# Optimization experiments

Measured on AMD Instinct MI355X. Metric: run time of the kernel, lower is better.

The kernel has to match this reference:

```python
import jax, jax.numpy as jnp
import numpy as np

B, S, D = 8, 2048, 512


def setup_inputs() -> dict:
    root = jax.random.key(0)
    kq, kk, kv, km = jax.random.split(root, 4)
    query = jax.random.normal(kq, (B, S, D), dtype=jnp.float32)
    key = jax.random.normal(kk, (B, S, D), dtype=jnp.float32)
    value = jax.random.normal(kv, (B, S, D), dtype=jnp.float32)
    # padding mask (batch, key_len): 1 = attend, 0 = masked. Force position 0
    # valid so no causal row is entirely masked (would yield NaN softmax).
    attention_mask = jax.random.randint(km, (B, S), 0, 2, dtype=jnp.int32).at[:, 0].set(1)
    return {"query": query, "key": key, "value": value, "attention_mask": attention_mask}


def reference(query, key, value, attention_mask):
    q_len, k_len = query.shape[1], key.shape[1]
    scale = 1.0 / jnp.sqrt(jnp.asarray(key.shape[-1], dtype=query.dtype))
    # [B, q_len, k_len] scores
    scores = jnp.einsum("bqd,bkd->bqk", query, key) * scale
    # causal (mask_future=True): lower-triangular allowed
    causal = jnp.tril(jnp.ones((q_len, k_len), dtype=bool))
    scores = jnp.where(causal[None, :, :], scores, -jnp.inf)
    # padding mask broadcast over query axis: (B, 1, k_len)
    scores = jnp.where(attention_mask[:, None, :] == 0, -jnp.inf, scores)
    probs = jax.nn.softmax(scores, axis=-1)
    return jnp.einsum("bqk,bkd->bqd", probs, value)
```

## Files before the change

kernel.cpp:

```cpp
#include <hip/hip_runtime.h>
#include <hip/hip_bf16.h>


typedef short bf16x8 __attribute__((ext_vector_type(8)));
typedef short s4v    __attribute__((ext_vector_type(4)));
typedef float f32x4  __attribute__((ext_vector_type(4)));
typedef float f4v    __attribute__((ext_vector_type(4)));
typedef float f2v    __attribute__((ext_vector_type(2)));
typedef unsigned int u32;

#define DEVINL __device__ __forceinline__

constexpr int kS = 2048;
constexpr int kD = 512;
constexpr int kB = 8;
constexpr int QT = 32;
constexpr int KROW = kD + 8;
constexpr float kC = 1.4426950408889634f * 0.044194173824159216f;
constexpr size_t kSlotB = (size_t)64 * kD * 2 + 64 * 4;

DEVINL float fast_exp2(float x) {
  float r; asm("v_exp_f32 %0, %1" : "=v"(r) : "v"(x)); return r;
}
DEVINL short f2b(float f) {
  return (short)__builtin_bit_cast(unsigned short, __float2bfloat16(f));
}
DEVINL f32x4 mfma16(bf16x8 a, bf16x8 b, f32x4 c) {
  return __builtin_amdgcn_mfma_f32_16x16x32_bf16(a, b, c, 0, 0, 0);
}
DEVINL void gl_lds16(const void* g, void* l) {
  __builtin_amdgcn_global_load_lds(
      (const __attribute__((address_space(1))) u32*)g,
      (__attribute__((address_space(3))) u32*)l, 16, 0, 0);
}
DEVINL float bflo(u32 u) { return __builtin_bit_cast(float, u << 16); }
DEVINL float bfhi(u32 u) { return __builtin_bit_cast(float, u & 0xffff0000u); }

template <int CTRL>
DEVINL float mvdpp(float x) {
  return __builtin_bit_cast(float,
      __builtin_amdgcn_mov_dpp(__builtin_bit_cast(int, x), CTRL, 0xf, 0xf, false));
}
DEVINL float rowsum16(float x) {
  x += mvdpp<0x128>(x);
  x += mvdpp<0x124>(x);
  x += mvdpp<0x122>(x);
  x += mvdpp<0x121>(x);
  return x;
}

__host__ __device__ __forceinline__ int ncM(int q, int TT) {
  return (2 * q + 2 + TT - 1) / TT;
}

__global__ __launch_bounds__(256) void prep(
    const float* __restrict__ K, const float* __restrict__ V,
    short* __restrict__ Kb, short* __restrict__ Vt) {
  __shared__ float Tl[64][65];
  const int blk = blockIdx.x;
  if (blk < 1024) {
    const size_t n4 = (size_t)kB * kS * kD / 4;
    for (size_t i = (size_t)blk * 256 + threadIdx.x; i < n4;
         i += (size_t)1024 * 256) {
      f4v v = *(const f4v*)(K + i * 4);
      s4v o = {f2b(v[0]), f2b(v[1]), f2b(v[2]), f2b(v[3])};
      *(s4v*)(Kb + i * 4) = o;
    }
  } else {
    const int r = blk - 1024;
    const int b = r >> 8, rr = r & 255;
    const int s0 = (rr >> 3) * 64, d0 = (rr & 7) * 64;
    const int t = threadIdx.x;
#pragma unroll
    for (int i = 0; i < 4; ++i) {
      int v = t + i * 256;
      int row = v >> 4, cq = v & 15;
      f4v x = *(const f4v*)(V + ((size_t)(b * kS + s0 + row)) * kD + d0 + cq * 4);
      *(f4v*)&Tl[row][cq * 4] = x;
    }
    __syncthreads();
    const int dd = t >> 2, q = t & 3;
    short out[16];
#pragma unroll
    for (int j = 0; j < 16; ++j) out[j] = f2b(Tl[q * 16 + j][dd]);
    short* dp = Vt + ((size_t)(b * kD + d0 + dd)) * kS + s0 + q * 16;
    *(bf16x8*)dp = *(const bf16x8*)&out[0];
    *(bf16x8*)(dp + 8) = *(const bf16x8*)&out[8];
  }
}

__global__ __launch_bounds__(256, 2) void attn_p1(
    const float* __restrict__ Qp, const short* __restrict__ Kb,
    const short* __restrict__ Vt, const int* __restrict__ Mp,
    float* __restrict__ Op, char* __restrict__ Part, int TT, int NS) {
  __shared__ __align__(16) short Klds[32 * 512];
  __shared__ __align__(16) short Vlds[128 * 128];
  __shared__ __align__(16) short Plds[64 * 40];
  __shared__ float Llds[64];
  __shared__ unsigned char Mlds[kS];

  const int tid = threadIdx.x, lane = tid & 63, w = tid >> 6;
  const int b = blockIdx.x & 7;

  int j = blockIdx.x >> 3;
  int sub = 0, qt = 0;
  for (;;) {
    const int qmin = (sub * TT) >> 1;
    const int cnt = QT - qmin;
    if (j < cnt) { qt = (QT - 1) - j; break; }
    j -= cnt;
    ++sub;
  }
  const int nc = ncM(qt, TT);
  const int ntl = 2 * qt + 2;
  const int t0 = sub * TT, t1 = min(ntl, t0 + TT);
  const int qbase = qt * 64;

  for (int i = tid; i < kS; i += 256) Mlds[i] = (unsigned char)Mp[(size_t)b * kS + i];

  const int l15 = lane & 15, lg = lane >> 4;

  bf16x8 qa[16];
  {
    const float* qp = Qp + ((size_t)(b * kS) + qbase + w * 16 + l15) * kD + lg * 8;
#pragma unroll
    for (int k = 0; k < 16; ++k) {
      f4v a = *(const f4v*)(qp + k * 32);
      f4v c = *(const f4v*)(qp + k * 32 + 4);
      bf16x8 q8 = {f2b(a[0]), f2b(a[1]), f2b(a[2]), f2b(a[3]),
                   f2b(c[0]), f2b(c[1]), f2b(c[2]), f2b(c[3])};
      qa[k] = q8;
    }
  }

  f32x4 acc[4][8];
#pragma unroll
  for (int qb = 0; qb < 4; ++qb)
#pragma unroll
    for (int db = 0; db < 8; ++db) acc[qb][db] = f32x4{0.f, 0.f, 0.f, 0.f};
  float lsum[4] = {0.f, 0.f, 0.f, 0.f};

  const int kx4 = (l15 >> 2) & 1;
  const short* kbase2 = &Klds[l15 * 512 + ((lg ^ (l15 & 3)) << 3)];
  const short* kpE = kbase2 + (kx4 << 5);
  const short* kpO = kbase2 - (kx4 << 5);
  const int vcom = (l15 >> 2) * 128 + ((l15 >> 1) & 1) * 64 + ((lg ^ (l15 >> 2)) << 3);
  const short* vE = &Vlds[vcom + (l15 & 1) * 32];
  const short* vO = &Vlds[vcom + ((l15 & 1) ^ 1) * 32];

  for (int t = t0; t < t1; ++t) {
    const int kv0 = t * 32;
    __syncthreads();

    {
      const short* kb = Kb + ((size_t)(b * kS) + kv0) * kD;
      const short* vt = Vt + (size_t)(b * kD) * kS + kv0;
      const int li = lane & 15, lh = lane >> 4;
#pragma unroll
      for (int r8 = 0; r8 < 8; ++r8) {
        const int row = w * 8 + r8;
        gl_lds16(kb + (size_t)row * kD + ((lane ^ (row & 7)) << 3),
                 &Klds[row * 512]);
      }
#pragma unroll
      for (int r8 = 0; r8 < 8; ++r8) {
        const int i = w * 8 + r8;
        const int sr = 4 * i + lh;
        const int logical = li ^ (4 * (i & 1) + lh);
        const int d = sr * 4 + (logical >> 2);
        gl_lds16(vt + (size_t)d * kS + ((logical & 3) << 3), &Vlds[i * 512]);
      }
    }
    __syncthreads();

    f32x4 sA = {0.f,0.f,0.f,0.f}, sB = {0.f,0.f,0.f,0.f};
    f32x4 sC = {0.f,0.f,0.f,0.f}, sD = {0.f,0.f,0.f,0.f};
    __builtin_amdgcn_s_setprio(1);
#pragma unroll
    for (int k = 0; k < 16; k += 2) {
      const short* pa = kpE + (k << 5);
      const short* pb = kpO + ((k + 1) << 5);
      bf16x8 b00 = *(const bf16x8*)(pa);
      bf16x8 b10 = *(const bf16x8*)(pa + 16 * 512);
      bf16x8 b01 = *(const bf16x8*)(pb);
      bf16x8 b11 = *(const bf16x8*)(pb + 16 * 512);
      sA = mfma16(qa[k], b00, sA);
      sB = mfma16(qa[k], b10, sB);
      sC = mfma16(qa[k + 1], b01, sC);
      sD = mfma16(qa[k + 1], b11, sD);
    }
    __builtin_amdgcn_s_setprio(0);
    f32x4 s0 = sA + sC;
    f32x4 s1 = sB + sD;

    const int kvg0 = kv0 + l15, kvg1 = kvg0 + 16;
    const int mk0 = Mlds[kvg0], mk1 = Mlds[kvg1];
    const int qrow0 = qbase + w * 16 + lg * 4;
#pragma unroll
    for (int jx = 0; jx < 4; ++jx) {
      const int q = qrow0 + jx;
      float x0 = (kvg0 <= q && mk0 != 0) ? s0[jx] : -1e30f;
      float x1 = (kvg1 <= q && mk1 != 0) ? s1[jx] : -1e30f;
      float p0 = fast_exp2(x0 * kC);
      float p1 = fast_exp2(x1 * kC);
      lsum[jx] += rowsum16(p0 + p1);
      Plds[(w * 16 + lg * 4 + jx) * 40 + l15]      = f2b(p0);
      Plds[(w * 16 + lg * 4 + jx) * 40 + 16 + l15] = f2b(p1);
    }
    __syncthreads();

    __builtin_amdgcn_s_setprio(1);
#pragma unroll
    for (int half = 0; half < 2; ++half) {
      bf16x8 vf[4];
#pragma unroll
      for (int i = 0; i < 4; ++i) {
        const int dc = 8 * w + half * 4 + i;
        vf[i] = (i & 1) ? *(const bf16x8*)(vO + dc * 512)
                        : *(const bf16x8*)(vE + dc * 512);
      }
#pragma unroll
      for (int qb = 0; qb < 4; ++qb) {
        bf16x8 pa = *(const bf16x8*)&Plds[(qb * 16 + l15) * 40 + lg * 8];
#pragma unroll
        for (int i = 0; i < 4; ++i)
          acc[qb][half * 4 + i] = mfma16(pa, vf[i], acc[qb][half * 4 + i]);
      }
    }
    __builtin_amdgcn_s_setprio(0);
  }

  __syncthreads();
  if (l15 == 0) {
    f32x4 lv = {lsum[0], lsum[1], lsum[2], lsum[3]};
    *(f32x4*)&Llds[w * 16 + lg * 4] = lv;
  }
  __syncthreads();

  if (nc == 1) {
#pragma unroll
    for (int qb = 0; qb < 4; ++qb) {
      f32x4 lv = *(const f32x4*)&Llds[qb * 16 + lg * 4];
#pragma unroll
      for (int jx = 0; jx < 4; ++jx) {
        const float inv = __builtin_amdgcn_rcpf(lv[jx]);
        const int row = qbase + qb * 16 + lg * 4 + jx;
        float* op = Op + ((size_t)(b * kS) + row) * kD + w * 128 + l15;
#pragma unroll
        for (int db = 0; db < 8; ++db) op[db * 16] = acc[qb][db][jx] * inv;
      }
    }
  } else {
    int sb = 0;
    for (int q = 0; q < qt; ++q) {
      int n2 = ncM(q, TT);
      if (n2 > 1) sb += n2;
    }
    char* sp = Part + ((size_t)b * NS + sb + sub) * kSlotB;
    short* po = (short*)sp;
    float* pm = (float*)(sp + (size_t)64 * kD * 2);
#pragma unroll
    for (int qb = 0; qb < 4; ++qb) {
#pragma unroll
      for (int jx = 0; jx < 4; ++jx) {
        const int row = qb * 16 + lg * 4 + jx;
#pragma unroll
        for (int db = 0; db < 8; ++db)
          po[row * kD + w * 128 + db * 16 + l15] = f2b(acc[qb][db][jx]);
      }
    }
    if (l15 == 0) {
#pragma unroll
      for (int jx = 0; jx < 4; ++jx) pm[w * 16 + lg * 4 + jx] = lsum[jx];
    }
  }
}

__global__ __launch_bounds__(256) void attn_p2(const char* __restrict__ Part,
                                               float* __restrict__ Op,
                                               int TT, int NS) {
  const int bid = blockIdx.x;
  const int b = bid & 7, rg = (bid >> 3) & 7, idx = bid >> 6;
  int seen = 0, qt = 0, nc = 0, sbase = 0, sb = 0;
  for (int q = 0; q < QT; ++q) {
    int n2 = ncM(q, TT);
    if (n2 > 1) {
      if (seen == idx) { qt = q; nc = n2; sbase = sb; break; }
      seen++;
      sb += n2;
    }
  }
  const int t = threadIdx.x;
  const char* base = Part + ((size_t)b * NS + sbase) * kSlotB;
  const int r0 = rg * 8;
  for (int row = r0; row < r0 + 8; ++row) {
    float lt = 0.f;
    for (int c = 0; c < nc; ++c)
      lt += *(const float*)(base + c * kSlotB + 65536 + row * 4);
    const float inv = 1.0f / lt;
    float a0 = 0.f, a1 = 0.f;
    for (int c = 0; c < nc; ++c) {
      u32 u = *(const u32*)(base + c * kSlotB + ((size_t)row * kD + t * 2) * 2);
      a0 += bflo(u);
      a1 += bfhi(u);
    }
    f2v o = {a0 * inv, a1 * inv};
    *(f2v*)(Op + ((size_t)(b * kS) + qt * 64 + row) * kD + t * 2) = o;
  }
}

__global__ __launch_bounds__(256) void attn_legacy(
    const float* __restrict__ Qp, const float* __restrict__ Kp,
    const float* __restrict__ Vp, const int* __restrict__ Mp,
    float* __restrict__ Op) {
  __shared__ __align__(16) short Klds[32 * KROW];
  __shared__ __align__(16) short Vlds[32 * kD];
  __shared__ __align__(16) short Plds[4 * 16 * 40];
  __shared__ int Mlds[kS];
  const int tid = threadIdx.x, lane = tid & 63, w = tid >> 6;
  const int bb = blockIdx.x & 7, qt = blockIdx.x >> 3, qb = qt * 64;
  for (int i = tid; i < kS; i += 256) Mlds[i] = Mp[(size_t)bb * kS + i];
  const int l15 = lane & 15, lg = lane >> 4;
  bf16x8 qa[16];
  {
    const float* qp = Qp + ((size_t)bb * kS + qb + w * 16 + l15) * kD + lg * 8;
#pragma unroll
    for (int k = 0; k < 16; ++k) {
      f4v a = *(const f4v*)(qp + k * 32);
      f4v c = *(const f4v*)(qp + k * 32 + 4);
      bf16x8 q8 = {f2b(a[0]), f2b(a[1]), f2b(a[2]), f2b(a[3]),
                   f2b(c[0]), f2b(c[1]), f2b(c[2]), f2b(c[3])};
      qa[k] = q8;
    }
  }
  f32x4 acc[32];
#pragma unroll
  for (int dc = 0; dc < 32; ++dc) acc[dc] = f32x4{0.f, 0.f, 0.f, 0.f};
  float mrow[4] = {-1e30f, -1e30f, -1e30f, -1e30f};
  float lsum[4] = {0.f, 0.f, 0.f, 0.f};
  short* Pl = &Plds[w * 16 * 40];
  const int vphys = ((lg ^ ((lane >> 2) & 3)) * 16);
  const int nt = 2 * qt + 2;
  for (int t = 0; t < nt; ++t) {
    const int kv0 = t * 32;
    __syncthreads();
    {
      const int r = tid >> 3, dg = tid & 7;
      const float* src = Kp + ((size_t)bb * kS + kv0 + r) * kD + dg * 64;
      short* dst = &Klds[r * KROW + dg * 64];
#pragma unroll
      for (int i = 0; i < 16; ++i) {
        f4v v = *(const f4v*)(src + i * 4);
        s4v s = {f2b(v[0]), f2b(v[1]), f2b(v[2]), f2b(v[3])};
        *(s4v*)(dst + i * 4) = s;
      }
    }
    {
      const int kvq = tid & 7, dqi = tid >> 3;
      const float* vbase = Vp + ((size_t)bb * kS + kv0 + kvq * 4) * kD;
#pragma unroll
      for (int it = 0; it < 4; ++it) {
        const int dq = dqi + 32 * it;
        f4v v0 = *(const f4v*)(vbase + 0 * kD + dq * 4);
        f4v v1 = *(const f4v*)(vbase + 1 * kD + dq * 4);
        f4v v2 = *(const f4v*)(vbase + 2 * kD + dq * 4);
        f4v v3 = *(const f4v*)(vbase + 3 * kD + dq * 4);
        const int pch = (((kvq >> 1) ^ (dq & 3)) * 16) + (kvq & 1) * 8;
#pragma unroll
        for (int c = 0; c < 4; ++c) {
          s4v s = {f2b(v0[c]), f2b(v1[c]), f2b(v2[c]), f2b(v3[c])};
          *(s4v*)((char*)Vlds + (dq * 4 + c) * 64 + pch) = s;
        }
      }
    }
    __syncthreads();
    f32x4 sA = {0.f,0.f,0.f,0.f}, sB = {0.f,0.f,0.f,0.f};
    f32x4 sC = {0.f,0.f,0.f,0.f}, sD = {0.f,0.f,0.f,0.f};
    const short* krow0 = &Klds[l15 * KROW + lg * 8];
    const short* krow1 = krow0 + 16 * KROW;
#pragma unroll
    for (int k = 0; k < 16; k += 2) {
      bf16x8 b00 = *(const bf16x8*)(krow0 + k * 32);
      bf16x8 b10 = *(const bf16x8*)(krow1 + k * 32);
      bf16x8 b01 = *(const bf16x8*)(krow0 + (k + 1) * 32);
      bf16x8 b11 = *(const bf16x8*)(krow1 + (k + 1) * 32);
      sA = mfma16(qa[k], b00, sA);
      sB = mfma16(qa[k], b10, sB);
      sC = mfma16(qa[k + 1], b01, sC);
      sD = mfma16(qa[k + 1], b11, sD);
    }
    f32x4 s0 = sA + sC, s1 = sB + sD;
    const int kvg0 = kv0 + l15, kvg1 = kvg0 + 16;
    const int mk0 = Mlds[kvg0], mk1 = Mlds[kvg1];
    const int qrow0 = qb + w * 16 + lg * 4;
    float rm[4];
#pragma unroll
    for (int jx = 0; jx < 4; ++jx) {
      const int q = qrow0 + jx;
      float x0 = (kvg0 <= q && mk0 != 0) ? s0[jx] : -1e30f;
      float x1 = (kvg1 <= q && mk1 != 0) ? s1[jx] : -1e30f;
      s0[jx] = x0; s1[jx] = x1;
      rm[jx] = fmaxf(x0, x1);
    }
#pragma unroll
    for (int sh = 1; sh <= 8; sh <<= 1) {
#pragma unroll
      for (int jx = 0; jx < 4; ++jx) rm[jx] = fmaxf(rm[jx], __shfl_xor(rm[jx], sh));
    }
    bool need = false;
#pragma unroll
    for (int jx = 0; jx < 4; ++jx) need |= ((rm[jx] - mrow[jx]) * kC > 8.0f);
    if (__any(need)) {
#pragma unroll
      for (int jx = 0; jx < 4; ++jx) {
        float mn = fmaxf(mrow[jx], rm[jx]);
        float corr = fast_exp2((mrow[jx] - mn) * kC);
        mrow[jx] = mn;
        lsum[jx] *= corr;
#pragma unroll
        for (int dc = 0; dc < 32; ++dc) acc[dc][jx] *= corr;
      }
    }
    float ts[4];
#pragma unroll
    for (int jx = 0; jx < 4; ++jx) {
      float p0 = fast_exp2((s0[jx] - mrow[jx]) * kC);
      float p1 = fast_exp2((s1[jx] - mrow[jx]) * kC);
      ts[jx] = p0 + p1;
      Pl[(lg * 4 + jx) * 40 + l15]      = f2b(p0);
      Pl[(lg * 4 + jx) * 40 + 16 + l15] = f2b(p1);
    }
#pragma unroll
    for (int sh = 1; sh <= 8; sh <<= 1) {
#pragma unroll
      for (int jx = 0; jx < 4; ++jx) ts[jx] += __shfl_xor(ts[jx], sh);
    }
#pragma unroll
    for (int jx = 0; jx < 4; ++jx) lsum[jx] += ts[jx];
    bf16x8 pf = *(const bf16x8*)&Pl[l15 * 40 + lg * 8];
#pragma unroll
    for (int dc = 0; dc < 32; ++dc) {
      const bf16x8 vf = *(const bf16x8*)((const char*)Vlds + (dc * 16 + l15) * 64 + vphys);
      acc[dc] = mfma16(pf, vf, acc[dc]);
    }
  }
#pragma unroll
  for (int jx = 0; jx < 4; ++jx) {
    const float inv = __builtin_amdgcn_rcpf(lsum[jx]);
    float* op = Op + ((size_t)bb * kS + qb + w * 16 + lg * 4 + jx) * kD + l15;
#pragma unroll
    for (int dc = 0; dc < 32; ++dc) op[dc * 16] = acc[dc][jx] * inv;
  }
}

extern "C" void kernel_launch(void* const* d_in, const int* in_sizes, int n_in,
                              void* d_out, int out_size, void* d_ws, size_t ws_size,
                              hipStream_t stream) {
  const float* Q = (const float*)d_in[0];
  const float* K = (const float*)d_in[1];
  const float* V = (const float*)d_in[2];
  const int*   M = (const int*)d_in[3];
  float* O = (float*)d_out;

  const size_t tens = (size_t)kB * kS * kD;
  const size_t convB = 2 * tens * 2;

  if (ws_size < convB) {
    attn_legacy<<<dim3(256), dim3(256), 0, stream>>>(Q, K, V, M, O);
    return;
  }

  short* Kb = (short*)d_ws;
  short* Vt = Kb + tens;
  char* Part = (char*)d_ws + convB;
  const size_t budget = ws_size - convB;

  int TT = 68;
  {
    const int cands[5] = {12, 16, 22, 34, 48};
    for (int ci = 0; ci < 5; ++ci) {
      int tt = cands[ci], slots = 0;
      for (int q = 0; q < QT; ++q) {
        int nc = ncM(q, tt);
        if (nc > 1) slots += nc;
      }
      if ((size_t)kB * slots * kSlotB <= budget) { TT = tt; break; }
    }
  }
  int NS = 0, NCH = 0, nsplit = 0;
  for (int q = 0; q < QT; ++q) {
    int nc = ncM(q, TT);
    NCH += nc;
    if (nc > 1) { NS += nc; nsplit++; }
  }

  prep<<<dim3(3072), dim3(256), 0, stream>>>(K, V, Kb, Vt);
  attn_p1<<<dim3(kB * NCH), dim3(256), 0, stream>>>(Q, Kb, Vt, M, O, Part, TT, NS);
  if (nsplit > 0)
    attn_p2<<<dim3(kB * 8 * nsplit), dim3(256), 0, stream>>>(Part, O, TT, NS);
}
```

Measured before the change: 180.4 us.

## Shrink query tile to 32 rows, split head dim across waves, share K/V LDS

The attention kernel now processes 32-query tiles instead of 64. The four waves are arranged as 2 query blocks by 2 head-dim halves, and the partial QK scores from the two halves are exchanged through a small LDS buffer. K and V now share one LDS buffer, loaded one after the other within each tile iteration, with explicit waitcnt and barriers. The mask is read from global memory instead of being staged in LDS. This cuts LDS usage so three blocks fit per CU and gives finer work granularity, at the cost of more barriers per tile, bf16 rounding of the exchanged partial scores, and twice the K/V tile loads per query.

```diff
diff --git a/kernel.cpp b/kernel.cpp
--- a/kernel.cpp
+++ b/kernel.cpp
@@ -8,16 +8,17 @@
 typedef float f4v    __attribute__((ext_vector_type(4)));
 typedef float f2v    __attribute__((ext_vector_type(2)));
 typedef unsigned int u32;
+typedef unsigned short u16;
 
 #define DEVINL __device__ __forceinline__
 
 constexpr int kS = 2048;
 constexpr int kD = 512;
 constexpr int kB = 8;
-constexpr int QT = 32;
+constexpr int QT3 = 64;
 constexpr int KROW = kD + 8;
 constexpr float kC = 1.4426950408889634f * 0.044194173824159216f;
-constexpr size_t kSlotB = (size_t)64 * kD * 2 + 64 * 4;
+constexpr size_t kSlot3 = (size_t)32 * kD * 2 + 32 * 4;
 
 DEVINL float fast_exp2(float x) {
   float r; asm("v_exp_f32 %0, %1" : "=v"(r) : "v"(x)); return r;
@@ -25,6 +26,7 @@
 DEVINL short f2b(float f) {
   return (short)__builtin_bit_cast(unsigned short, __float2bfloat16(f));
 }
+DEVINL float b2f(u16 u) { return __builtin_bit_cast(float, (u32)u << 16); }
 DEVINL f32x4 mfma16(bf16x8 a, bf16x8 b, f32x4 c) {
   return __builtin_amdgcn_mfma_f32_16x16x32_bf16(a, b, c, 0, 0, 0);
 }
@@ -49,8 +51,8 @@
   return x;
 }
 
-__host__ __device__ __forceinline__ int ncM(int q, int TT) {
-  return (2 * q + 2 + TT - 1) / TT;
+__host__ __device__ __forceinline__ int nc3(int qt, int TT) {
+  return (qt + 1 + TT - 1) / TT;
 }
 
 __global__ __launch_bounds__(256) void prep(
@@ -89,42 +91,39 @@
   }
 }
 
-__global__ __launch_bounds__(256, 2) void attn_p1(
+__global__ __launch_bounds__(256, 3) void attn_p1(
     const float* __restrict__ Qp, const short* __restrict__ Kb,
     const short* __restrict__ Vt, const int* __restrict__ Mp,
     float* __restrict__ Op, char* __restrict__ Part, int TT, int NS) {
-  __shared__ __align__(16) short Klds[32 * 512];
-  __shared__ __align__(16) short Vlds[128 * 128];
-  __shared__ __align__(16) short Plds[64 * 40];
-  __shared__ float Llds[64];
-  __shared__ unsigned char Mlds[kS];
+  __shared__ __align__(16) short KV[32 * 512];
+  __shared__ __align__(16) short Plds[32 * 40];
+  __shared__ __align__(16) short Slds[2][2][16][32];
 
   const int tid = threadIdx.x, lane = tid & 63, w = tid >> 6;
+  const int qb2 = w & 1, dh = w >> 1;
   const int b = blockIdx.x & 7;
 
-  int j = blockIdx.x >> 3;
-  int sub = 0, qt = 0;
+  int j = blockIdx.x >> 3, sub = 0, qt = 0;
   for (;;) {
-    const int qmin = (sub * TT) >> 1;
-    const int cnt = QT - qmin;
-    if (j < cnt) { qt = (QT - 1) - j; break; }
+    const int qmin = sub * TT;
+    const int cnt = QT3 - qmin;
+    if (j < cnt) { qt = (QT3 - 1) - j; break; }
     j -= cnt;
     ++sub;
   }
-  const int nc = ncM(qt, TT);
-  const int ntl = 2 * qt + 2;
+  const int ntl = qt + 1;
+  const int nc = nc3(qt, TT);
   const int t0 = sub * TT, t1 = min(ntl, t0 + TT);
-  const int qbase = qt * 64;
-
-  for (int i = tid; i < kS; i += 256) Mlds[i] = (unsigned char)Mp[(size_t)b * kS + i];
+  const int qbase = qt * 32;
 
   const int l15 = lane & 15, lg = lane >> 4;
 
-  bf16x8 qa[16];
+  bf16x8 qa[8];
   {
-    const float* qp = Qp + ((size_t)(b * kS) + qbase + w * 16 + l15) * kD + lg * 8;
-#pragma unroll
-    for (int k = 0; k < 16; ++k) {
+    const float* qp =
+        Qp + ((size_t)(b * kS) + qbase + qb2 * 16 + l15) * kD + dh * 256 + lg * 8;
+#pragma unroll
+    for (int k = 0; k < 8; ++k) {
       f4v a = *(const f4v*)(qp + k * 32);
       f4v c = *(const f4v*)(qp + k * 32 + 4);
       bf16x8 q8 = {f2b(a[0]), f2b(a[1]), f2b(a[2]), f2b(a[3]),
@@ -133,51 +132,47 @@
     }
   }
 
-  f32x4 acc[4][8];
-#pragma unroll
-  for (int qb = 0; qb < 4; ++qb)
-#pragma unroll
-    for (int db = 0; db < 8; ++db) acc[qb][db] = f32x4{0.f, 0.f, 0.f, 0.f};
+  f32x4 acc[16];
+#pragma unroll
+  for (int dc = 0; dc < 16; ++dc) acc[dc] = f32x4{0.f, 0.f, 0.f, 0.f};
   float lsum[4] = {0.f, 0.f, 0.f, 0.f};
 
   const int kx4 = (l15 >> 2) & 1;
-  const short* kbase2 = &Klds[l15 * 512 + ((lg ^ (l15 & 3)) << 3)];
+  const short* kbase2 = &KV[l15 * 512 + dh * 256 + ((lg ^ (l15 & 3)) << 3)];
   const short* kpE = kbase2 + (kx4 << 5);
   const short* kpO = kbase2 - (kx4 << 5);
   const int vcom = (l15 >> 2) * 128 + ((l15 >> 1) & 1) * 64 + ((lg ^ (l15 >> 2)) << 3);
-  const short* vE = &Vlds[vcom + (l15 & 1) * 32];
-  const short* vO = &Vlds[vcom + ((l15 & 1) ^ 1) * 32];
+  const short* vE = &KV[vcom + (l15 & 1) * 32];
+  const short* vO = &KV[vcom + ((l15 & 1) ^ 1) * 32];
+
+  const short* kbG = Kb + (size_t)(b * kS) * kD;
+  const short* vtG = Vt + (size_t)(b * kD) * kS;
+  const int* mp = Mp + (size_t)b * kS;
 
   for (int t = t0; t < t1; ++t) {
     const int kv0 = t * 32;
-    __syncthreads();
+
+    __builtin_amdgcn_s_barrier();
+    __builtin_amdgcn_sched_barrier(0);
 
     {
-      const short* kb = Kb + ((size_t)(b * kS) + kv0) * kD;
-      const short* vt = Vt + (size_t)(b * kD) * kS + kv0;
-      const int li = lane & 15, lh = lane >> 4;
+      const short* kb = kbG + (size_t)kv0 * kD;
 #pragma unroll
       for (int r8 = 0; r8 < 8; ++r8) {
         const int row = w * 8 + r8;
         gl_lds16(kb + (size_t)row * kD + ((lane ^ (row & 7)) << 3),
-                 &Klds[row * 512]);
-      }
-#pragma unroll
-      for (int r8 = 0; r8 < 8; ++r8) {
-        const int i = w * 8 + r8;
-        const int sr = 4 * i + lh;
-        const int logical = li ^ (4 * (i & 1) + lh);
-        const int d = sr * 4 + (logical >> 2);
-        gl_lds16(vt + (size_t)d * kS + ((logical & 3) << 3), &Vlds[i * 512]);
-      }
-    }
-    __syncthreads();
+                 &KV[row * 512]);
+      }
+    }
+    asm volatile("s_waitcnt vmcnt(0)" ::: "memory");
+    __builtin_amdgcn_s_barrier();
+    __builtin_amdgcn_sched_barrier(0);
 
     f32x4 sA = {0.f,0.f,0.f,0.f}, sB = {0.f,0.f,0.f,0.f};
     f32x4 sC = {0.f,0.f,0.f,0.f}, sD = {0.f,0.f,0.f,0.f};
     __builtin_amdgcn_s_setprio(1);
 #pragma unroll
-    for (int k = 0; k < 16; k += 2) {
+    for (int k = 0; k < 8; k += 2) {
       const short* pa = kpE + (k << 5);
       const short* pb = kpO + ((k + 1) << 5);
       bf16x8 b00 = *(const bf16x8*)(pa);
@@ -190,88 +185,96 @@
       sD = mfma16(qa[k + 1], b11, sD);
     }
     __builtin_amdgcn_s_setprio(0);
-    f32x4 s0 = sA + sC;
-    f32x4 s1 = sB + sD;
-
-    const int kvg0 = kv0 + l15, kvg1 = kvg0 + 16;
-    const int mk0 = Mlds[kvg0], mk1 = Mlds[kvg1];
-    const int qrow0 = qbase + w * 16 + lg * 4;
+    f32x4 s0p = sA + sC;
+    f32x4 s1p = sB + sD;
+
 #pragma unroll
     for (int jx = 0; jx < 4; ++jx) {
-      const int q = qrow0 + jx;
-      float x0 = (kvg0 <= q && mk0 != 0) ? s0[jx] : -1e30f;
-      float x1 = (kvg1 <= q && mk1 != 0) ? s1[jx] : -1e30f;
-      float p0 = fast_exp2(x0 * kC);
-      float p1 = fast_exp2(x1 * kC);
-      lsum[jx] += rowsum16(p0 + p1);
-      Plds[(w * 16 + lg * 4 + jx) * 40 + l15]      = f2b(p0);
-      Plds[(w * 16 + lg * 4 + jx) * 40 + 16 + l15] = f2b(p1);
-    }
-    __syncthreads();
-
+      Slds[qb2][dh][lg * 4 + jx][l15]      = f2b(s0p[jx]);
+      Slds[qb2][dh][lg * 4 + jx][l15 + 16] = f2b(s1p[jx]);
+    }
+    asm volatile("s_waitcnt lgkmcnt(0)" ::: "memory");
+    __builtin_amdgcn_s_barrier();
+    __builtin_amdgcn_sched_barrier(0);
+
+    {
+      const short* vt = vtG + kv0;
+      const int li = lane & 15, lh = lane >> 4;
+#pragma unroll
+      for (int r8 = 0; r8 < 8; ++r8) {
+        const int i = w * 8 + r8;
+        const int sr = 4 * i + lh;
+        const int logical = li ^ (4 * (i & 1) + lh);
+        const int d = sr * 4 + (logical >> 2);
+        gl_lds16(vt + (size_t)d * kS + ((logical & 3) << 3), &KV[i * 512]);
+      }
+    }
+
+    {
+      const int kvg0 = kv0 + l15, kvg1 = kvg0 + 16;
+      const int mk0 = mp[kvg0], mk1 = mp[kvg1];
+      const int qrow0 = qbase + qb2 * 16 + lg * 4;
+#pragma unroll
+      for (int jx = 0; jx < 4; ++jx) {
+        const int row = lg * 4 + jx;
+        const float o0 = b2f((u16)Slds[qb2][dh ^ 1][row][l15]);
+        const float o1 = b2f((u16)Slds[qb2][dh ^ 1][row][l15 + 16]);
+        float x0 = s0p[jx] + o0;
+        float x1 = s1p[jx] + o1;
+        const int q = qrow0 + jx;
+        x0 = (kvg0 <= q && mk0 != 0) ? x0 : -1e30f;
+        x1 = (kvg1 <= q && mk1 != 0) ? x1 : -1e30f;
+        const float p0 = fast_exp2(x0 * kC);
+        const float p1 = fast_exp2(x1 * kC);
+        lsum[jx] += rowsum16(p0 + p1);
+        if (dh == 0) {
+          Plds[(qb2 * 16 + row) * 40 + l15]      = f2b(p0);
+          Plds[(qb2 * 16 + row) * 40 + 16 + l15] = f2b(p1);
+        }
+      }
+    }
+    asm volatile("s_waitcnt vmcnt(0) lgkmcnt(0)" ::: "memory");
+    __builtin_amdgcn_s_barrier();
+    __builtin_amdgcn_sched_barrier(0);
+
+    bf16x8 pa = *(const bf16x8*)&Plds[(qb2 * 16 + l15) * 40 + lg * 8];
     __builtin_amdgcn_s_setprio(1);
 #pragma unroll
-    for (int half = 0; half < 2; ++half) {
-      bf16x8 vf[4];
-#pragma unroll
-      for (int i = 0; i < 4; ++i) {
-        const int dc = 8 * w + half * 4 + i;
-        vf[i] = (i & 1) ? *(const bf16x8*)(vO + dc * 512)
-                        : *(const bf16x8*)(vE + dc * 512);
-      }
-#pragma unroll
-      for (int qb = 0; qb < 4; ++qb) {
-        bf16x8 pa = *(const bf16x8*)&Plds[(qb * 16 + l15) * 40 + lg * 8];
-#pragma unroll
-        for (int i = 0; i < 4; ++i)
-          acc[qb][half * 4 + i] = mfma16(pa, vf[i], acc[qb][half * 4 + i]);
-      }
+    for (int dc2 = 0; dc2 < 16; dc2 += 2) {
+      const int dcA = dh * 16 + dc2;
+      bf16x8 vf0 = *(const bf16x8*)(vE + dcA * 512);
+      bf16x8 vf1 = *(const bf16x8*)(vO + (dcA + 1) * 512);
+      acc[dc2]     = mfma16(pa, vf0, acc[dc2]);
+      acc[dc2 + 1] = mfma16(pa, vf1, acc[dc2 + 1]);
     }
     __builtin_amdgcn_s_setprio(0);
   }
 
-  __syncthreads();
-  if (l15 == 0) {
-    f32x4 lv = {lsum[0], lsum[1], lsum[2], lsum[3]};
-    *(f32x4*)&Llds[w * 16 + lg * 4] = lv;
-  }
-  __syncthreads();
-
   if (nc == 1) {
 #pragma unroll
-    for (int qb = 0; qb < 4; ++qb) {
-      f32x4 lv = *(const f32x4*)&Llds[qb * 16 + lg * 4];
-#pragma unroll
-      for (int jx = 0; jx < 4; ++jx) {
-        const float inv = __builtin_amdgcn_rcpf(lv[jx]);
-        const int row = qbase + qb * 16 + lg * 4 + jx;
-        float* op = Op + ((size_t)(b * kS) + row) * kD + w * 128 + l15;
-#pragma unroll
-        for (int db = 0; db < 8; ++db) op[db * 16] = acc[qb][db][jx] * inv;
-      }
+    for (int jx = 0; jx < 4; ++jx) {
+      const float inv = __builtin_amdgcn_rcpf(lsum[jx]);
+      const int row = qbase + qb2 * 16 + lg * 4 + jx;
+      float* op = Op + ((size_t)(b * kS) + row) * kD + dh * 256 + l15;
+#pragma unroll
+      for (int dc = 0; dc < 16; ++dc) op[dc * 16] = acc[dc][jx] * inv;
     }
   } else {
     int sb = 0;
     for (int q = 0; q < qt; ++q) {
-      int n2 = ncM(q, TT);
+      int n2 = nc3(q, TT);
       if (n2 > 1) sb += n2;
     }
-    char* sp = Part + ((size_t)b * NS + sb + sub) * kSlotB;
+    char* sp = Part + ((size_t)b * NS + sb + sub) * kSlot3;
     short* po = (short*)sp;
-    float* pm = (float*)(sp + (size_t)64 * kD * 2);
-#pragma unroll
-    for (int qb = 0; qb < 4; ++qb) {
-#pragma unroll
-      for (int jx = 0; jx < 4; ++jx) {
-        const int row = qb * 16 + lg * 4 + jx;
-#pragma unroll
-        for (int db = 0; db < 8; ++db)
-          po[row * kD + w * 128 + db * 16 + l15] = f2b(acc[qb][db][jx]);
-      }
-    }
-    if (l15 == 0) {
-#pragma unroll
-      for (int jx = 0; jx < 4; ++jx) pm[w * 16 + lg * 4 + jx] = lsum[jx];
+    float* pm = (float*)(sp + (size_t)32 * kD * 2);
+#pragma unroll
+    for (int jx = 0; jx < 4; ++jx) {
+      const int row = qb2 * 16 + lg * 4 + jx;
+#pragma unroll
+      for (int dc = 0; dc < 16; ++dc)
+        po[row * kD + dh * 256 + dc * 16 + l15] = f2b(acc[dc][jx]);
+      if (dh == 0 && l15 == 0) pm[row] = lsum[jx];
     }
   }
 }
@@ -280,10 +283,10 @@
                                                float* __restrict__ Op,
                                                int TT, int NS) {
   const int bid = blockIdx.x;
-  const int b = bid & 7, rg = (bid >> 3) & 7, idx = bid >> 6;
+  const int b = bid & 7, rg = (bid >> 3) & 3, idx = bid >> 5;
   int seen = 0, qt = 0, nc = 0, sbase = 0, sb = 0;
-  for (int q = 0; q < QT; ++q) {
-    int n2 = ncM(q, TT);
+  for (int q = 0; q < QT3; ++q) {
+    int n2 = nc3(q, TT);
     if (n2 > 1) {
       if (seen == idx) { qt = q; nc = n2; sbase = sb; break; }
       seen++;
@@ -291,21 +294,21 @@
     }
   }
   const int t = threadIdx.x;
-  const char* base = Part + ((size_t)b * NS + sbase) * kSlotB;
+  const char* base = Part + ((size_t)b * NS + sbase) * kSlot3;
   const int r0 = rg * 8;
   for (int row = r0; row < r0 + 8; ++row) {
     float lt = 0.f;
     for (int c = 0; c < nc; ++c)
-      lt += *(const float*)(base + c * kSlotB + 65536 + row * 4);
+      lt += *(const float*)(base + c * kSlot3 + 32768 + row * 4);
     const float inv = 1.0f / lt;
     float a0 = 0.f, a1 = 0.f;
     for (int c = 0; c < nc; ++c) {
-      u32 u = *(const u32*)(base + c * kSlotB + ((size_t)row * kD + t * 2) * 2);
+      u32 u = *(const u32*)(base + c * kSlot3 + ((size_t)row * kD + t * 2) * 2);
       a0 += bflo(u);
       a1 += bfhi(u);
     }
     f2v o = {a0 * inv, a1 * inv};
-    *(f2v*)(Op + ((size_t)(b * kS) + qt * 64 + row) * kD + t * 2) = o;
+    *(f2v*)(Op + ((size_t)(b * kS) + qt * 32 + row) * kD + t * 2) = o;
   }
 }
 
@@ -475,21 +478,21 @@
   char* Part = (char*)d_ws + convB;
   const size_t budget = ws_size - convB;
 
-  int TT = 68;
+  int TT = QT3;
   {
-    const int cands[5] = {12, 16, 22, 34, 48};
-    for (int ci = 0; ci < 5; ++ci) {
+    const int cands[4] = {16, 24, 32, 48};
+    for (int ci = 0; ci < 4; ++ci) {
       int tt = cands[ci], slots = 0;
-      for (int q = 0; q < QT; ++q) {
-        int nc = ncM(q, tt);
+      for (int q = 0; q < QT3; ++q) {
+        int nc = nc3(q, tt);
         if (nc > 1) slots += nc;
       }
-      if ((size_t)kB * slots * kSlotB <= budget) { TT = tt; break; }
+      if ((size_t)kB * slots * kSlot3 <= budget) { TT = tt; break; }
     }
   }
   int NS = 0, NCH = 0, nsplit = 0;
-  for (int q = 0; q < QT; ++q) {
-    int nc = ncM(q, TT);
+  for (int q = 0; q < QT3; ++q) {
+    int nc = nc3(q, TT);
     NCH += nc;
     if (nc > 1) { NS += nc; nsplit++; }
   }
@@ -497,5 +500,5 @@
   prep<<<dim3(3072), dim3(256), 0, stream>>>(K, V, Kb, Vt);
   attn_p1<<<dim3(kB * NCH), dim3(256), 0, stream>>>(Q, Kb, Vt, M, O, Part, TT, NS);
   if (nsplit > 0)
-    attn_p2<<<dim3(kB * 8 * nsplit), dim3(256), 0, stream>>>(Part, O, TT, NS);
-}
+    attn_p2<<<dim3(kB * 4 * nsplit), dim3(256), 0, stream>>>(Part, O, TT, NS);
+}
```

Result: slower. 238.9 us (+32.4%).

## Split QK^T over head-dim halves and prefetch K/V tiles across barriers

Applied to the files above, without the earlier changes.

Each wave now computes QK^T for 32 query rows over half of the head dimension and exchanges partial scores through a small LDS buffer, so every K fragment read from LDS feeds two query blocks. K for the next tile is staged while the softmax runs, and V is staged during QK^T, using explicit waitcnt and barrier ordering in place of __syncthreads. The mask is read straight from global memory instead of being staged in LDS. This adds an extra LDS round-trip and barrier for the partial-sum exchange, and relies on hand-counted vmcnt values being correct.

```diff
diff --git a/kernel.cpp b/kernel.cpp
--- a/kernel.cpp
+++ b/kernel.cpp
@@ -8,6 +8,7 @@
 typedef float f4v    __attribute__((ext_vector_type(4)));
 typedef float f2v    __attribute__((ext_vector_type(2)));
 typedef unsigned int u32;
+typedef unsigned short u16;
 
 #define DEVINL __device__ __forceinline__
 
@@ -96,14 +97,14 @@
   __shared__ __align__(16) short Klds[32 * 512];
   __shared__ __align__(16) short Vlds[128 * 128];
   __shared__ __align__(16) short Plds[64 * 40];
+  __shared__ float Slds[2][2][16][33];
   __shared__ float Llds[64];
-  __shared__ unsigned char Mlds[kS];
 
   const int tid = threadIdx.x, lane = tid & 63, w = tid >> 6;
+  const int qh = w & 1, dh = w >> 1;
   const int b = blockIdx.x & 7;
 
-  int j = blockIdx.x >> 3;
-  int sub = 0, qt = 0;
+  int j = blockIdx.x >> 3, sub = 0, qt = 0;
   for (;;) {
     const int qmin = (sub * TT) >> 1;
     const int cnt = QT - qmin;
@@ -116,20 +117,50 @@
   const int t0 = sub * TT, t1 = min(ntl, t0 + TT);
   const int qbase = qt * 64;
 
-  for (int i = tid; i < kS; i += 256) Mlds[i] = (unsigned char)Mp[(size_t)b * kS + i];
-
   const int l15 = lane & 15, lg = lane >> 4;
-
-  bf16x8 qa[16];
+  const short* kbG = Kb + (size_t)(b * kS) * kD;
+  const short* vtG = Vt + (size_t)(b * kD) * kS;
+  const int* mp = Mp + (size_t)b * kS;
+
+  auto stageK = [&](int t) {
+    const short* kb = kbG + (size_t)(t * 32) * kD;
+#pragma unroll
+    for (int r8 = 0; r8 < 8; ++r8) {
+      const int row = w * 8 + r8;
+      gl_lds16(kb + (size_t)row * kD + ((lane ^ (row & 7)) << 3),
+               &Klds[row * 512]);
+    }
+  };
+  auto stageV = [&](int t) {
+    const short* vt = vtG + t * 32;
+    const int li = lane & 15, lh = lane >> 4;
+#pragma unroll
+    for (int r8 = 0; r8 < 8; ++r8) {
+      const int i = w * 8 + r8;
+      const int sr = 4 * i + lh;
+      const int logical = li ^ (4 * (i & 1) + lh);
+      const int d = sr * 4 + (logical >> 2);
+      gl_lds16(vt + (size_t)d * kS + ((logical & 3) << 3), &Vlds[i * 512]);
+    }
+  };
+
+  stageK(t0);
+
+  bf16x8 qa[2][8];
   {
-    const float* qp = Qp + ((size_t)(b * kS) + qbase + w * 16 + l15) * kD + lg * 8;
-#pragma unroll
-    for (int k = 0; k < 16; ++k) {
-      f4v a = *(const f4v*)(qp + k * 32);
-      f4v c = *(const f4v*)(qp + k * 32 + 4);
-      bf16x8 q8 = {f2b(a[0]), f2b(a[1]), f2b(a[2]), f2b(a[3]),
-                   f2b(c[0]), f2b(c[1]), f2b(c[2]), f2b(c[3])};
-      qa[k] = q8;
+#pragma unroll
+    for (int qrb = 0; qrb < 2; ++qrb) {
+      const float* qp = Qp +
+          ((size_t)(b * kS) + qbase + qh * 32 + qrb * 16 + l15) * kD +
+          dh * 256 + lg * 8;
+#pragma unroll
+      for (int k = 0; k < 8; ++k) {
+        f4v a = *(const f4v*)(qp + k * 32);
+        f4v c = *(const f4v*)(qp + k * 32 + 4);
+        bf16x8 q8 = {f2b(a[0]), f2b(a[1]), f2b(a[2]), f2b(a[3]),
+                     f2b(c[0]), f2b(c[1]), f2b(c[2]), f2b(c[3])};
+        qa[qrb][k] = q8;
+      }
     }
   }
 
@@ -141,7 +172,7 @@
   float lsum[4] = {0.f, 0.f, 0.f, 0.f};
 
   const int kx4 = (l15 >> 2) & 1;
-  const short* kbase2 = &Klds[l15 * 512 + ((lg ^ (l15 & 3)) << 3)];
+  const short* kbase2 = &Klds[l15 * 512 + dh * 256 + ((lg ^ (l15 & 3)) << 3)];
   const short* kpE = kbase2 + (kx4 << 5);
   const short* kpO = kbase2 - (kx4 << 5);
   const int vcom = (l15 >> 2) * 128 + ((l15 >> 1) & 1) * 64 + ((lg ^ (l15 >> 2)) << 3);
@@ -150,64 +181,81 @@
 
   for (int t = t0; t < t1; ++t) {
     const int kv0 = t * 32;
-    __syncthreads();
-
-    {
-      const short* kb = Kb + ((size_t)(b * kS) + kv0) * kD;
-      const short* vt = Vt + (size_t)(b * kD) * kS + kv0;
-      const int li = lane & 15, lh = lane >> 4;
-#pragma unroll
-      for (int r8 = 0; r8 < 8; ++r8) {
-        const int row = w * 8 + r8;
-        gl_lds16(kb + (size_t)row * kD + ((lane ^ (row & 7)) << 3),
-                 &Klds[row * 512]);
-      }
-#pragma unroll
-      for (int r8 = 0; r8 < 8; ++r8) {
-        const int i = w * 8 + r8;
-        const int sr = 4 * i + lh;
-        const int logical = li ^ (4 * (i & 1) + lh);
-        const int d = sr * 4 + (logical >> 2);
-        gl_lds16(vt + (size_t)d * kS + ((logical & 3) << 3), &Vlds[i * 512]);
-      }
-    }
-    __syncthreads();
-
-    f32x4 sA = {0.f,0.f,0.f,0.f}, sB = {0.f,0.f,0.f,0.f};
-    f32x4 sC = {0.f,0.f,0.f,0.f}, sD = {0.f,0.f,0.f,0.f};
+
+    asm volatile("s_waitcnt vmcnt(0)" ::: "memory");
+    __builtin_amdgcn_s_barrier();
+    __builtin_amdgcn_sched_barrier(0);
+
+    stageV(t);
+
+    f32x4 s00 = {0,0,0,0}, s01 = {0,0,0,0}, s10 = {0,0,0,0}, s11 = {0,0,0,0};
     __builtin_amdgcn_s_setprio(1);
 #pragma unroll
-    for (int k = 0; k < 16; k += 2) {
+    for (int k = 0; k < 8; k += 2) {
       const short* pa = kpE + (k << 5);
       const short* pb = kpO + ((k + 1) << 5);
       bf16x8 b00 = *(const bf16x8*)(pa);
       bf16x8 b10 = *(const bf16x8*)(pa + 16 * 512);
       bf16x8 b01 = *(const bf16x8*)(pb);
       bf16x8 b11 = *(const bf16x8*)(pb + 16 * 512);
-      sA = mfma16(qa[k], b00, sA);
-      sB = mfma16(qa[k], b10, sB);
-      sC = mfma16(qa[k + 1], b01, sC);
-      sD = mfma16(qa[k + 1], b11, sD);
+      s00 = mfma16(qa[0][k], b00, s00);
+      s10 = mfma16(qa[1][k], b00, s10);
+      s01 = mfma16(qa[0][k], b10, s01);
+      s11 = mfma16(qa[1][k], b10, s11);
+      s00 = mfma16(qa[0][k + 1], b01, s00);
+      s10 = mfma16(qa[1][k + 1], b01, s10);
+      s01 = mfma16(qa[0][k + 1], b11, s01);
+      s11 = mfma16(qa[1][k + 1], b11, s11);
     }
     __builtin_amdgcn_s_setprio(0);
-    f32x4 s0 = sA + sC;
-    f32x4 s1 = sB + sD;
-
-    const int kvg0 = kv0 + l15, kvg1 = kvg0 + 16;
-    const int mk0 = Mlds[kvg0], mk1 = Mlds[kvg1];
-    const int qrow0 = qbase + w * 16 + lg * 4;
-#pragma unroll
-    for (int jx = 0; jx < 4; ++jx) {
-      const int q = qrow0 + jx;
-      float x0 = (kvg0 <= q && mk0 != 0) ? s0[jx] : -1e30f;
-      float x1 = (kvg1 <= q && mk1 != 0) ? s1[jx] : -1e30f;
-      float p0 = fast_exp2(x0 * kC);
-      float p1 = fast_exp2(x1 * kC);
-      lsum[jx] += rowsum16(p0 + p1);
-      Plds[(w * 16 + lg * 4 + jx) * 40 + l15]      = f2b(p0);
-      Plds[(w * 16 + lg * 4 + jx) * 40 + 16 + l15] = f2b(p1);
-    }
-    __syncthreads();
+
+    {
+      const f32x4 x0 = (dh == 0) ? s10 : s00;
+      const f32x4 x1 = (dh == 0) ? s11 : s01;
+      const int reg = dh ^ 1;
+#pragma unroll
+      for (int jx = 0; jx < 4; ++jx) {
+        Slds[dh][qh][lg * 4 + jx][l15]          = x0[jx];
+        Slds[dh][qh][lg * 4 + jx][l15 + 16]     = x1[jx];
+      }
+      (void)reg;
+    }
+    asm volatile("s_waitcnt lgkmcnt(0)" ::: "memory");
+    __builtin_amdgcn_s_barrier();
+    __builtin_amdgcn_sched_barrier(0);
+
+    if (t + 1 < t1) stageK(t + 1);
+
+    {
+      f32x4 o0 = (dh == 0) ? s00 : s10;
+      f32x4 o1 = (dh == 0) ? s01 : s11;
+      const int kvg0 = kv0 + l15, kvg1 = kvg0 + 16;
+      const int mk0 = mp[kvg0], mk1 = mp[kvg1];
+      const int qrow0 = qbase + qh * 32 + dh * 16 + lg * 4;
+#pragma unroll
+      for (int jx = 0; jx < 4; ++jx) {
+        const float p0p = Slds[dh ^ 1][qh][lg * 4 + jx][l15];
+        const float p1p = Slds[dh ^ 1][qh][lg * 4 + jx][l15 + 16];
+        float x0 = o0[jx] + p0p;
+        float x1 = o1[jx] + p1p;
+        const int q = qrow0 + jx;
+        x0 = (kvg0 <= q && mk0 != 0) ? x0 : -1e30f;
+        x1 = (kvg1 <= q && mk1 != 0) ? x1 : -1e30f;
+        const float p0 = fast_exp2(x0 * kC);
+        const float p1 = fast_exp2(x1 * kC);
+        lsum[jx] += rowsum16(p0 + p1);
+        const int row = qh * 32 + dh * 16 + lg * 4 + jx;
+        Plds[row * 40 + l15]      = f2b(p0);
+        Plds[row * 40 + 16 + l15] = f2b(p1);
+      }
+    }
+    if (t + 1 < t1) {
+      asm volatile("s_waitcnt vmcnt(8) lgkmcnt(0)" ::: "memory");
+    } else {
+      asm volatile("s_waitcnt vmcnt(0) lgkmcnt(0)" ::: "memory");
+    }
+    __builtin_amdgcn_s_barrier();
+    __builtin_amdgcn_sched_barrier(0);
 
     __builtin_amdgcn_s_setprio(1);
 #pragma unroll
@@ -233,7 +281,7 @@
   __syncthreads();
   if (l15 == 0) {
     f32x4 lv = {lsum[0], lsum[1], lsum[2], lsum[3]};
-    *(f32x4*)&Llds[w * 16 + lg * 4] = lv;
+    *(f32x4*)&Llds[qh * 32 + dh * 16 + lg * 4] = lv;
   }
   __syncthreads();
 
@@ -271,7 +319,8 @@
     }
     if (l15 == 0) {
 #pragma unroll
-      for (int jx = 0; jx < 4; ++jx) pm[w * 16 + lg * 4 + jx] = lsum[jx];
+      for (int jx = 0; jx < 4; ++jx)
+        pm[qh * 32 + dh * 16 + lg * 4 + jx] = lsum[jx];
     }
   }
 }
```

New measurement: 218.6 us. 1.21x slower.

## Prefetch next K/V tile into registers to overlap global loads with compute

Applied to the files above, without the earlier changes.

Replaces the direct global-to-LDS loads of each K/V tile with register staging. The next tile is fetched into registers while the current tile is computed, then written to LDS at the next iteration's barrier. This is meant to hide global memory latency behind the MFMA and softmax work. It costs 16 extra bf16x8 registers per thread, which could lower occupancy or cause spills under launch_bounds(256,2), and it relies on hand-placed waitcnts and barriers.

```diff
diff --git a/kernel.cpp b/kernel.cpp
--- a/kernel.cpp
+++ b/kernel.cpp
@@ -27,11 +27,6 @@
 }
 DEVINL f32x4 mfma16(bf16x8 a, bf16x8 b, f32x4 c) {
   return __builtin_amdgcn_mfma_f32_16x16x32_bf16(a, b, c, 0, 0, 0);
-}
-DEVINL void gl_lds16(const void* g, void* l) {
-  __builtin_amdgcn_global_load_lds(
-      (const __attribute__((address_space(1))) u32*)g,
-      (__attribute__((address_space(3))) u32*)l, 16, 0, 0);
 }
 DEVINL float bflo(u32 u) { return __builtin_bit_cast(float, u << 16); }
 DEVINL float bfhi(u32 u) { return __builtin_bit_cast(float, u & 0xffff0000u); }
@@ -102,8 +97,7 @@
   const int tid = threadIdx.x, lane = tid & 63, w = tid >> 6;
   const int b = blockIdx.x & 7;
 
-  int j = blockIdx.x >> 3;
-  int sub = 0, qt = 0;
+  int j = blockIdx.x >> 3, sub = 0, qt = 0;
   for (;;) {
     const int qmin = (sub * TT) >> 1;
     const int cnt = QT - qmin;
@@ -119,6 +113,41 @@
   for (int i = tid; i < kS; i += 256) Mlds[i] = (unsigned char)Mp[(size_t)b * kS + i];
 
   const int l15 = lane & 15, lg = lane >> 4;
+  const short* kbG = Kb + (size_t)(b * kS) * kD;
+  const short* vtG = Vt + (size_t)(b * kD) * kS;
+
+  bf16x8 kreg[8], vreg[8];
+  auto loadKV = [&](int t) {
+    const short* kb = kbG + (size_t)(t * 32) * kD;
+    const short* vt = vtG + t * 32;
+#pragma unroll
+    for (int r8 = 0; r8 < 8; ++r8) {
+      const int row = w * 8 + r8;
+      kreg[r8] = *(const bf16x8*)(kb + (size_t)row * kD + ((lane ^ (row & 7)) << 3));
+    }
+#pragma unroll
+    for (int r8 = 0; r8 < 8; ++r8) {
+      const int i = w * 8 + r8;
+      const int sr = 4 * i + lg;
+      const int logical = l15 ^ (4 * (i & 1) + lg);
+      const int d = sr * 4 + (logical >> 2);
+      vreg[r8] = *(const bf16x8*)(vt + (size_t)d * kS + ((logical & 3) << 3));
+    }
+  };
+  auto writeKV = [&]() {
+#pragma unroll
+    for (int r8 = 0; r8 < 8; ++r8) {
+      const int row = w * 8 + r8;
+      *(bf16x8*)&Klds[row * 512 + lane * 8] = kreg[r8];
+    }
+#pragma unroll
+    for (int r8 = 0; r8 < 8; ++r8) {
+      const int i = w * 8 + r8;
+      *(bf16x8*)&Vlds[i * 512 + lane * 8] = vreg[r8];
+    }
+  };
+
+  loadKV(t0);
 
   bf16x8 qa[16];
   {
@@ -150,28 +179,15 @@
 
   for (int t = t0; t < t1; ++t) {
     const int kv0 = t * 32;
-    __syncthreads();
-
-    {
-      const short* kb = Kb + ((size_t)(b * kS) + kv0) * kD;
-      const short* vt = Vt + (size_t)(b * kD) * kS + kv0;
-      const int li = lane & 15, lh = lane >> 4;
-#pragma unroll
-      for (int r8 = 0; r8 < 8; ++r8) {
-        const int row = w * 8 + r8;
-        gl_lds16(kb + (size_t)row * kD + ((lane ^ (row & 7)) << 3),
-                 &Klds[row * 512]);
-      }
-#pragma unroll
-      for (int r8 = 0; r8 < 8; ++r8) {
-        const int i = w * 8 + r8;
-        const int sr = 4 * i + lh;
-        const int logical = li ^ (4 * (i & 1) + lh);
-        const int d = sr * 4 + (logical >> 2);
-        gl_lds16(vt + (size_t)d * kS + ((logical & 3) << 3), &Vlds[i * 512]);
-      }
-    }
-    __syncthreads();
+
+    __builtin_amdgcn_s_barrier();
+    __builtin_amdgcn_sched_barrier(0);
+    asm volatile("s_waitcnt vmcnt(0)" ::: "memory");
+    writeKV();
+    if (t + 1 < t1) loadKV(t + 1);
+    asm volatile("s_waitcnt lgkmcnt(0)" ::: "memory");
+    __builtin_amdgcn_s_barrier();
+    __builtin_amdgcn_sched_barrier(0);
 
     f32x4 sA = {0.f,0.f,0.f,0.f}, sB = {0.f,0.f,0.f,0.f};
     f32x4 sC = {0.f,0.f,0.f,0.f}, sD = {0.f,0.f,0.f,0.f};
```

After: 352.2 us. 1.95x slower.
